# Performance work log

Hardware: AMD Instinct MI355X
Metric: run time of the kernel (lower is better)

## Reference

```python
import jax, jax.numpy as jnp
import numpy as np

BETA = 0.25  # commitment loss coefficient


def setup_inputs() -> dict:
    key = jax.random.key(0)
    kx, kc = jax.random.split(key)
    # x: [B, T, D] latents; codebooks: [M, K, D] (equal K per level -> stacked)
    x = jax.random.normal(kx, (64, 1024, 256), dtype=jnp.float32)
    # small init akin to RandomUniform(-1/K, 1/K)
    codebooks = jax.random.normal(kc, (4, 1024, 256), dtype=jnp.float32) * (1.0 / 1024.0)
    return {"x": x, "codebooks": codebooks}


def reference(x, codebooks):
    """Residual VQ forward (inference path: no EMA state update).

    Returns (y, commit_loss): y = x + stop_grad(sum_l q_l - x) (straight-through),
    commit_loss = beta * sum_l mean((stop_grad(q_l) - r_l)^2).
    """
    D = x.shape[-1]
    M = codebooks.shape[0]
    flat = x.reshape(-1, D)                      # [N, D]
    residual = flat
    q_sum = jnp.zeros_like(flat)
    commit = jnp.zeros((), dtype=x.dtype)
    for lvl in range(M):                         # M is small & fixed (4)
        cb = codebooks[lvl]                      # [K, D]
        # squared L2 distances: ||r||^2 + ||e||^2 - 2 r.e^T
        r2 = jnp.sum(residual * residual, axis=1, keepdims=True)   # [N, 1]
        e2 = jnp.sum(cb * cb, axis=1)                               # [K]
        dist = r2 + e2 - 2.0 * jnp.matmul(residual, cb.T)           # [N, K]
        idx = jnp.argmin(dist, axis=1)                              # [N]
        q = jnp.take(cb, idx, axis=0)                               # [N, D]
        q_st = jax.lax.stop_gradient(q)
        commit = commit + BETA * jnp.mean((q_st - residual) ** 2)
        q_sum = q_sum + q
        residual = residual - q_st
    y_flat = flat + jax.lax.stop_gradient(q_sum - flat)
    return y_flat.reshape(x.shape), commit
```

## Files before the change

kernel.cpp:

```cpp
#include <hip/hip_runtime.h>

#define DIM 256
#define KCODES 1024
#define LEVELS 4
#define CHUNK 64
#define NCHUNK 16
#define TOKB 128
#define NTOK 65536
#define NELEM (NTOK * DIM)

typedef _Float16 h8 __attribute__((ext_vector_type(8)));
typedef _Float16 h4 __attribute__((ext_vector_type(4)));
typedef _Float16 h2 __attribute__((ext_vector_type(2)));
typedef float f4 __attribute__((ext_vector_type(4)));
typedef float f16v __attribute__((ext_vector_type(16)));
typedef unsigned int u32;

__device__ __forceinline__ void gload16(const void* g, void* l) {
  __builtin_amdgcn_global_load_lds(
      (const __attribute__((address_space(1))) void*)g,
      (__attribute__((address_space(3))) void*)l, 16, 0, 0);
}

__device__ __forceinline__ float sq8(h8 r, float acc) {
#if __has_builtin(__builtin_amdgcn_fdot2)
  #pragma unroll
  for (int j = 0; j < 4; ++j) {
    h2 p = {r[2 * j], r[2 * j + 1]};
    acc = __builtin_amdgcn_fdot2(p, p, acc, false);
  }
#else
  #pragma unroll
  for (int j = 0; j < 8; ++j) { float v = (float)r[j]; acc += v * v; }
#endif
  return acc;
}

__global__ __launch_bounds__(256) void rvq_prep(const float* __restrict__ cb,
                                                _Float16* __restrict__ cb16,
                                                float* __restrict__ e2p,
                                                float* __restrict__ out) {
  if (blockIdx.x == 0 && threadIdx.x == 0) out[NELEM] = 0.0f;
  const int row = blockIdx.x * 4 + (threadIdx.x >> 6);
  const int lane = threadIdx.x & 63;
  const float* src = cb + (size_t)row * DIM + lane * 4;
  f4 v = *(const f4*)src;
  h4 hv;
  hv[0] = (_Float16)v[0]; hv[1] = (_Float16)v[1];
  hv[2] = (_Float16)v[2]; hv[3] = (_Float16)v[3];
  *(h4*)(cb16 + (size_t)row * DIM + lane * 4) = hv;
  float s = v[0]*v[0] + v[1]*v[1] + v[2]*v[2] + v[3]*v[3];
  #pragma unroll
  for (int off = 32; off; off >>= 1) s += __shfl_xor(s, off, 64);
  if (lane == 0) e2p[row] = 0.25f - 0.5f * s;
}

__global__ __launch_bounds__(128, 1) void rvq_main(
    const float* __restrict__ x, const float* __restrict__ cb32,
    const _Float16* __restrict__ cb16, const float* __restrict__ e2p,
    float* __restrict__ out) {
  __shared__ __attribute__((aligned(16))) _Float16 clds[2][CHUNK * DIM];
  __shared__ float e2_lds[KCODES];
  __shared__ __attribute__((aligned(16))) int idx_hist[TOKB][4];
  __shared__ float r2_sh[TOKB];
  __shared__ float csum_sh[2];

  const int tid = threadIdx.x;
  const int wave = tid >> 6, lane = tid & 63;
  const int col = lane & 31, Lhi = lane >> 5;

  int soff[16];
  #pragma unroll
  for (int i = 0; i < 16; ++i) {
    const int rl = wave * 32 + 2 * i + Lhi;
    soff[i] = rl * 512 + ((col ^ (rl & 7)) << 4);
  }
  int swz4[4];
  #pragma unroll
  for (int m = 0; m < 4; ++m)
    swz4[m] = (((((m << 1) | Lhi) ^ col) & 7) << 4);

  const char* cb16b = (const char*)cb16;
  {
    char* ldst = (char*)&clds[0][0] + wave * 16384;
    #pragma unroll
    for (int i = 0; i < 16; ++i) gload16(cb16b + soff[i], ldst + i * 1024);
  }

  h8 af[2][16];
  float r2p[2] = {0.f, 0.f};
  const size_t tok0 = (size_t)blockIdx.x * TOKB + wave * 64;
  #pragma unroll
  for (int mt = 0; mt < 2; ++mt) {
    const float* xr = x + (tok0 + mt * 32 + col) * DIM + Lhi * 8;
    #pragma unroll
    for (int kk = 0; kk < 16; ++kk) {
      f4 a = *(const f4*)(xr + kk * 16);
      f4 b = *(const f4*)(xr + kk * 16 + 4);
      h8 h;
      #pragma unroll
      for (int j = 0; j < 4; ++j) { h[j] = (_Float16)a[j]; h[4 + j] = (_Float16)b[j]; }
      af[mt][kk] = h;
      r2p[mt] = sq8(h, r2p[mt]);
    }
  }

  float commit_acc = 0.f;

  for (int lvl = 0; lvl < LEVELS; ++lvl) {
    #pragma unroll
    for (int mt = 0; mt < 2; ++mt) {
      float s = r2p[mt] + __shfl_xor(r2p[mt], 32, 64);
      if (Lhi == 0) r2_sh[wave * 64 + mt * 32 + col] = s;
    }
    *(f4*)&e2_lds[tid * 8] = *(const f4*)(e2p + (lvl << 10) + tid * 8);
    *(f4*)&e2_lds[tid * 8 + 4] = *(const f4*)(e2p + (lvl << 10) + tid * 8 + 4);

    u32 best[2][16];
    #pragma unroll
    for (int mt = 0; mt < 2; ++mt)
      #pragma unroll
      for (int i = 0; i < 16; ++i) best[mt][i] = 0u;

    for (int c = 0; c < NCHUNK; ++c) {
      __syncthreads();
      {
        const int gn = lvl * NCHUNK + c + 1;
        const char* gsrc = cb16b + ((size_t)(gn < 64 ? gn : 63) << 15);
        char* ldst = (char*)&clds[(c + 1) & 1][0] + wave * 16384;
        #pragma unroll
        for (int i = 0; i < 16; ++i) gload16(gsrc + soff[i], ldst + i * 1024);
      }

      const char* cbuf = (const char*)&clds[c & 1][0] + col * 512;
      #pragma unroll
      for (int nt = 0; nt < 2; ++nt) {
        const int code0 = c * 64 + nt * 32;
        const float e2v = e2_lds[code0 + col];
        f16v acc0, acc1;
        #pragma unroll
        for (int i = 0; i < 16; ++i) { acc0[i] = e2v; acc1[i] = e2v; }
        #pragma unroll
        for (int kk = 0; kk < 16; ++kk) {
          h8 b = *(const h8*)(cbuf + nt * 16384 + swz4[kk & 3] + ((kk >> 2) << 7));
          acc0 = __builtin_amdgcn_mfma_f32_32x32x16_f16(af[0][kk], b, acc0, 0, 0, 0);
          acc1 = __builtin_amdgcn_mfma_f32_32x32x16_f16(af[1][kk], b, acc1, 0, 0, 0);
        }
        const u32 invc = (u32)(code0 + col) ^ 1023u;
        #pragma unroll
        for (int i = 0; i < 16; ++i) {
          u32 p0 = (__float_as_uint(acc0[i]) & 0xFFFFFC00u) | invc;
          if (p0 > best[0][i]) best[0][i] = p0;
          u32 p1 = (__float_as_uint(acc1[i]) & 0xFFFFFC00u) | invc;
          if (p1 > best[1][i]) best[1][i] = p1;
        }
      }
    }

    #pragma unroll
    for (int mt = 0; mt < 2; ++mt)
      #pragma unroll
      for (int i = 0; i < 16; ++i) {
        u32 b = best[mt][i];
        #pragma unroll
        for (int off = 1; off < 32; off <<= 1) {
          u32 o = __shfl_xor(b, off, 32);
          if (o > b) b = o;
        }
        best[mt][i] = b;
      }

    if (col == 0) {
      #pragma unroll
      for (int mt = 0; mt < 2; ++mt)
        #pragma unroll
        for (int i = 0; i < 16; ++i) {
          const u32 p = best[mt][i];
          const int code = (int)((p & 1023u) ^ 1023u);
          const int t = wave * 64 + mt * 32 + (i & 3) + 8 * (i >> 2) + 4 * Lhi;
          idx_hist[t][lvl] = code;
          const float sc = __uint_as_float(p & 0xFFFFFC00u) - 0.25f;
          commit_acc += r2_sh[t] - 2.0f * sc;
        }
    }
    __syncthreads();

    if (lvl < LEVELS - 1) {
      r2p[0] = 0.f; r2p[1] = 0.f;
      #pragma unroll
      for (int mt = 0; mt < 2; ++mt) {
        const int qidx = idx_hist[wave * 64 + mt * 32 + col][lvl];
        const _Float16* qr = cb16 + (((size_t)lvl << 10) + qidx) * DIM + Lhi * 8;
        #pragma unroll
        for (int kk = 0; kk < 16; ++kk) {
          h8 q = *(const h8*)(qr + kk * 16);
          h8 r = af[mt][kk] - q;
          af[mt][kk] = r;
          r2p[mt] = sq8(r, r2p[mt]);
        }
      }
    }
  }

  float* yblk = out + (size_t)blockIdx.x * (TOKB * DIM);
  #pragma unroll 4
  for (int it = 0; it < 64; ++it) {
    const int f = it * 512 + tid * 4;
    const int t = f >> 8;
    const int d = f & 255;
    const int4 qi = *(const int4*)&idx_hist[t][0];
    f4 q0 = *(const f4*)(cb32 + (size_t)qi.x * DIM + d);
    f4 q1 = *(const f4*)(cb32 + (size_t)(1024 + qi.y) * DIM + d);
    f4 q2 = *(const f4*)(cb32 + (size_t)(2048 + qi.z) * DIM + d);
    f4 q3 = *(const f4*)(cb32 + (size_t)(3072 + qi.w) * DIM + d);
    f4 y = (q0 + q1) + (q2 + q3);
    *(f4*)(yblk + f) = y;
  }

  #pragma unroll
  for (int off = 1; off < 64; off <<= 1) commit_acc += __shfl_xor(commit_acc, off, 64);
  if (lane == 0) csum_sh[wave] = commit_acc;
  __syncthreads();
  if (tid == 0) {
    const float tot = csum_sh[0] + csum_sh[1];
    atomicAdd(out + NELEM, tot * (0.25f / 16777216.0f));
  }
}

extern "C" void kernel_launch(void* const* d_in, const int* in_sizes, int n_in,
                              void* d_out, int out_size, void* d_ws, size_t ws_size,
                              hipStream_t stream) {
  const float* x = (const float*)d_in[0];
  const float* cb = (const float*)d_in[1];
  float* out = (float*)d_out;
  _Float16* cb16 = (_Float16*)d_ws;
  float* e2p = (float*)((char*)d_ws + (size_t)LEVELS * KCODES * DIM * sizeof(_Float16));

  rvq_prep<<<(LEVELS * KCODES) / 4, 256, 0, stream>>>(cb, cb16, e2p, out);
  rvq_main<<<NTOK / TOKB, 128, 0, stream>>>(x, cb, cb16, e2p, out);
}
```

Baseline: 299.4 us.

## Split each chunk's codes across wave pairs, doubling waves per block

The block grows from 2 to 4 waves. Each pair of waves shares the same 64 tokens and each wave handles half of every 64-code chunk, so each wave does half the MFMA work per chunk and the codebook loads are spread over more waves. The per-wave argmin results are merged through a new shared-memory exchange plus an extra barrier per level. Both waves in a pair recompute the residual update and keep duplicate A fragments in registers, so residual work and VGPR use are duplicated, in exchange for more latency hiding.

```diff
diff --git a/kernel.cpp b/kernel.cpp
--- a/kernel.cpp
+++ b/kernel.cpp
@@ -55,7 +55,7 @@
   if (lane == 0) e2p[row] = 0.25f - 0.5f * s;
 }
 
-__global__ __launch_bounds__(128, 1) void rvq_main(
+__global__ __launch_bounds__(256, 2) void rvq_main(
     const float* __restrict__ x, const float* __restrict__ cb32,
     const _Float16* __restrict__ cb16, const float* __restrict__ e2p,
     float* __restrict__ out) {
@@ -63,16 +63,18 @@
   __shared__ float e2_lds[KCODES];
   __shared__ __attribute__((aligned(16))) int idx_hist[TOKB][4];
   __shared__ float r2_sh[TOKB];
-  __shared__ float csum_sh[2];
+  __shared__ u32 bestsh[4][64];
+  __shared__ float csum_sh[4];
 
   const int tid = threadIdx.x;
   const int wave = tid >> 6, lane = tid & 63;
   const int col = lane & 31, Lhi = lane >> 5;
-
-  int soff[16];
-  #pragma unroll
-  for (int i = 0; i < 16; ++i) {
-    const int rl = wave * 32 + 2 * i + Lhi;
+  const int group = wave >> 1, half = wave & 1;
+
+  int soff[8];
+  #pragma unroll
+  for (int i = 0; i < 8; ++i) {
+    const int rl = wave * 16 + 2 * i + Lhi;
     soff[i] = rl * 512 + ((col ^ (rl & 7)) << 4);
   }
   int swz4[4];
@@ -82,14 +84,14 @@
 
   const char* cb16b = (const char*)cb16;
   {
-    char* ldst = (char*)&clds[0][0] + wave * 16384;
-    #pragma unroll
-    for (int i = 0; i < 16; ++i) gload16(cb16b + soff[i], ldst + i * 1024);
+    char* ldst = (char*)&clds[0][0] + wave * 8192;
+    #pragma unroll
+    for (int i = 0; i < 8; ++i) gload16(cb16b + soff[i], ldst + i * 1024);
   }
 
   h8 af[2][16];
   float r2p[2] = {0.f, 0.f};
-  const size_t tok0 = (size_t)blockIdx.x * TOKB + wave * 64;
+  const size_t tok0 = (size_t)blockIdx.x * TOKB + group * 64;
   #pragma unroll
   for (int mt = 0; mt < 2; ++mt) {
     const float* xr = x + (tok0 + mt * 32 + col) * DIM + Lhi * 8;
@@ -111,10 +113,9 @@
     #pragma unroll
     for (int mt = 0; mt < 2; ++mt) {
       float s = r2p[mt] + __shfl_xor(r2p[mt], 32, 64);
-      if (Lhi == 0) r2_sh[wave * 64 + mt * 32 + col] = s;
-    }
-    *(f4*)&e2_lds[tid * 8] = *(const f4*)(e2p + (lvl << 10) + tid * 8);
-    *(f4*)&e2_lds[tid * 8 + 4] = *(const f4*)(e2p + (lvl << 10) + tid * 8 + 4);
+      if (half == 0 && Lhi == 0) r2_sh[group * 64 + mt * 32 + col] = s;
+    }
+    *(f4*)&e2_lds[tid * 4] = *(const f4*)(e2p + (lvl << 10) + tid * 4);
 
     u32 best[2][16];
     #pragma unroll
@@ -127,33 +128,30 @@
       {
         const int gn = lvl * NCHUNK + c + 1;
         const char* gsrc = cb16b + ((size_t)(gn < 64 ? gn : 63) << 15);
-        char* ldst = (char*)&clds[(c + 1) & 1][0] + wave * 16384;
-        #pragma unroll
-        for (int i = 0; i < 16; ++i) gload16(gsrc + soff[i], ldst + i * 1024);
-      }
-
-      const char* cbuf = (const char*)&clds[c & 1][0] + col * 512;
-      #pragma unroll
-      for (int nt = 0; nt < 2; ++nt) {
-        const int code0 = c * 64 + nt * 32;
-        const float e2v = e2_lds[code0 + col];
-        f16v acc0, acc1;
-        #pragma unroll
-        for (int i = 0; i < 16; ++i) { acc0[i] = e2v; acc1[i] = e2v; }
-        #pragma unroll
-        for (int kk = 0; kk < 16; ++kk) {
-          h8 b = *(const h8*)(cbuf + nt * 16384 + swz4[kk & 3] + ((kk >> 2) << 7));
-          acc0 = __builtin_amdgcn_mfma_f32_32x32x16_f16(af[0][kk], b, acc0, 0, 0, 0);
-          acc1 = __builtin_amdgcn_mfma_f32_32x32x16_f16(af[1][kk], b, acc1, 0, 0, 0);
-        }
-        const u32 invc = (u32)(code0 + col) ^ 1023u;
-        #pragma unroll
-        for (int i = 0; i < 16; ++i) {
-          u32 p0 = (__float_as_uint(acc0[i]) & 0xFFFFFC00u) | invc;
-          if (p0 > best[0][i]) best[0][i] = p0;
-          u32 p1 = (__float_as_uint(acc1[i]) & 0xFFFFFC00u) | invc;
-          if (p1 > best[1][i]) best[1][i] = p1;
-        }
+        char* ldst = (char*)&clds[(c + 1) & 1][0] + wave * 8192;
+        #pragma unroll
+        for (int i = 0; i < 8; ++i) gload16(gsrc + soff[i], ldst + i * 1024);
+      }
+
+      const int code0 = c * 64 + half * 32;
+      const char* bptr = (const char*)&clds[c & 1][0] + (half * 32 + col) * 512;
+      const float e2v = e2_lds[code0 + col];
+      f16v acc0, acc1;
+      #pragma unroll
+      for (int i = 0; i < 16; ++i) { acc0[i] = e2v; acc1[i] = e2v; }
+      #pragma unroll
+      for (int kk = 0; kk < 16; ++kk) {
+        h8 b = *(const h8*)(bptr + swz4[kk & 3] + ((kk >> 2) << 7));
+        acc0 = __builtin_amdgcn_mfma_f32_32x32x16_f16(af[0][kk], b, acc0, 0, 0, 0);
+        acc1 = __builtin_amdgcn_mfma_f32_32x32x16_f16(af[1][kk], b, acc1, 0, 0, 0);
+      }
+      const u32 invc = (u32)(code0 + col) ^ 1023u;
+      #pragma unroll
+      for (int i = 0; i < 16; ++i) {
+        u32 p0 = (__float_as_uint(acc0[i]) & 0xFFFFFC00u) | invc;
+        if (p0 > best[0][i]) best[0][i] = p0;
+        u32 p1 = (__float_as_uint(acc1[i]) & 0xFFFFFC00u) | invc;
+        if (p1 > best[1][i]) best[1][i] = p1;
       }
     }
 
@@ -174,14 +172,22 @@
       #pragma unroll
       for (int mt = 0; mt < 2; ++mt)
         #pragma unroll
-        for (int i = 0; i < 16; ++i) {
-          const u32 p = best[mt][i];
-          const int code = (int)((p & 1023u) ^ 1023u);
-          const int t = wave * 64 + mt * 32 + (i & 3) + 8 * (i >> 2) + 4 * Lhi;
-          idx_hist[t][lvl] = code;
-          const float sc = __uint_as_float(p & 0xFFFFFC00u) - 0.25f;
-          commit_acc += r2_sh[t] - 2.0f * sc;
-        }
+        for (int i = 0; i < 16; ++i)
+          bestsh[wave][mt * 32 + i * 2 + Lhi] = best[mt][i];
+    }
+    __syncthreads();
+
+    if (half == 0) {
+      const int e = lane;
+      const int mt = e >> 5, i = (e >> 1) & 15, lh = e & 1;
+      u32 p0 = bestsh[group * 2 + 0][e];
+      u32 p1 = bestsh[group * 2 + 1][e];
+      const u32 p = p0 > p1 ? p0 : p1;
+      const int code = (int)((p & 1023u) ^ 1023u);
+      const int t = group * 64 + mt * 32 + (i & 3) + 8 * (i >> 2) + 4 * lh;
+      idx_hist[t][lvl] = code;
+      const float sc = __uint_as_float(p & 0xFFFFFC00u) - 0.25f;
+      commit_acc += r2_sh[t] - 2.0f * sc;
     }
     __syncthreads();
 
@@ -189,7 +195,7 @@
       r2p[0] = 0.f; r2p[1] = 0.f;
       #pragma unroll
       for (int mt = 0; mt < 2; ++mt) {
-        const int qidx = idx_hist[wave * 64 + mt * 32 + col][lvl];
+        const int qidx = idx_hist[group * 64 + mt * 32 + col][lvl];
         const _Float16* qr = cb16 + (((size_t)lvl << 10) + qidx) * DIM + Lhi * 8;
         #pragma unroll
         for (int kk = 0; kk < 16; ++kk) {
@@ -204,8 +210,8 @@
 
   float* yblk = out + (size_t)blockIdx.x * (TOKB * DIM);
   #pragma unroll 4
-  for (int it = 0; it < 64; ++it) {
-    const int f = it * 512 + tid * 4;
+  for (int it = 0; it < 32; ++it) {
+    const int f = it * 1024 + tid * 4;
     const int t = f >> 8;
     const int d = f & 255;
     const int4 qi = *(const int4*)&idx_hist[t][0];
@@ -222,7 +228,7 @@
   if (lane == 0) csum_sh[wave] = commit_acc;
   __syncthreads();
   if (tid == 0) {
-    const float tot = csum_sh[0] + csum_sh[1];
+    const float tot = csum_sh[0] + csum_sh[1] + csum_sh[2] + csum_sh[3];
     atomicAdd(out + NELEM, tot * (0.25f / 16777216.0f));
   }
 }
@@ -237,5 +243,5 @@
   float* e2p = (float*)((char*)d_ws + (size_t)LEVELS * KCODES * DIM * sizeof(_Float16));
 
   rvq_prep<<<(LEVELS * KCODES) / 4, 256, 0, stream>>>(cb, cb16, e2p, out);
-  rvq_main<<<NTOK / TOKB, 128, 0, stream>>>(x, cb, cb16, e2p, out);
-}
+  rvq_main<<<NTOK / TOKB, 256, 0, stream>>>(x, cb, cb16, e2p, out);
+}
```

After: 270.4 us. -9.7%, faster.
